# Kernel optimization log

Measured on AMD Instinct MI355X. Metric: run time of the kernel, lower is better.

## Reference

```python
import jax, jax.numpy as jnp
import numpy as np

N_NODES = 100000
N_EDGES = 1600000
N_GRAPHS = 64
D_IN = 64
D_HID = 64
D_OUT = 64


def gcn_conv(x, W, b, src, dst, n):
    """PyG-style GCNConv: x' = D^-1/2 (A+I) D^-1/2 (x W) + b."""
    xw = x @ W  # [N, d_out]
    loops = jnp.arange(n, dtype=src.dtype)
    s = jnp.concatenate([src, loops])  # add self-loops
    d = jnp.concatenate([dst, loops])
    deg = jax.ops.segment_sum(jnp.ones_like(d, dtype=xw.dtype), d, num_segments=n)
    dinv = jax.lax.rsqrt(jnp.maximum(deg, 1.0))
    coef = dinv[s] * dinv[d]  # [E+N]
    msg = xw[s] * coef[:, None]  # gather + scale, [E+N, d_out]
    out = jax.ops.segment_sum(msg, d, num_segments=n)  # scatter-add
    return out + b


def global_mean_pool(h, batch, num_graphs):
    sums = jax.ops.segment_sum(h, batch, num_segments=num_graphs)
    cnt = jax.ops.segment_sum(jnp.ones((h.shape[0],), h.dtype), batch, num_segments=num_graphs)
    return sums / jnp.maximum(cnt, 1.0)[:, None]


def setup_inputs() -> dict:
    key = jax.random.key(0)
    ks = jax.random.split(key, 8)
    x = jax.random.normal(ks[0], (N_NODES, D_IN), dtype=jnp.float32)
    edge_index = jax.random.randint(ks[1], (2, N_EDGES), 0, N_NODES, dtype=jnp.int64 if jax.config.jax_enable_x64 else jnp.int32)
    batch = jnp.sort(jax.random.randint(ks[2], (N_NODES,), 0, N_GRAPHS))
    sc = lambda fan_in: 1.0 / np.sqrt(fan_in)
    W1 = jax.random.uniform(ks[3], (D_IN, D_HID), jnp.float32, -sc(D_IN), sc(D_IN))
    b1 = jnp.zeros((D_HID,), jnp.float32)
    W2 = jax.random.uniform(ks[4], (D_HID, D_HID), jnp.float32, -sc(D_HID), sc(D_HID))
    b2 = jnp.zeros((D_HID,), jnp.float32)
    Wp = jax.random.uniform(ks[5], (D_HID, D_OUT), jnp.float32, -sc(D_HID), sc(D_HID))
    bp = jax.random.uniform(ks[6], (D_OUT,), jnp.float32, -sc(D_HID), sc(D_HID))
    return {"x": x, "edge_index": edge_index, "batch": batch,
            "W1": W1, "b1": b1, "W2": W2, "b2": b2, "Wp": Wp, "bp": bp}


def reference(x, edge_index, batch, W1, b1, W2, b2, Wp, bp):
    src, dst = edge_index[0], edge_index[1]
    n = x.shape[0]
    h = jax.nn.relu(gcn_conv(x, W1, b1, src, dst, n))
    h = jax.nn.relu(gcn_conv(h, W2, b2, src, dst, n))
    hg = global_mean_pool(h, batch, N_GRAPHS)  # [G, d_hid]
    return hg @ Wp + bp  # [G, d_out]
```

## Files before the change

### kernel.cpp

```cpp
#include <hip/hip_runtime.h>
#include <hip/hip_fp16.h>


#define DF 64
#define BSH 7
#define BNODES 128
#define CAP 4096

struct alignas(8)  h4 { __half2 a, b; };
struct alignas(16) h8 { __half2 a, b, c, d; };


__global__ __launch_bounds__(256) void part_kernel(
        const int* __restrict__ src, const int* __restrict__ dst,
        const int4* __restrict__ src4, const int4* __restrict__ dst4,
        int E, unsigned* __restrict__ bedges, int* __restrict__ bucketCur, int nb) {
    __shared__ int lcnt[1024];
    __shared__ int lbase[1024];
    int tid = threadIdx.x;
    for (int t = tid; t < nb; t += 256) lcnt[t] = 0;
    __syncthreads();
    int nq = E >> 2;
    unsigned packed[32];
    int bkt[32];
    int rk[32];
    int qbase = blockIdx.x * 2048;
#pragma unroll
    for (int c = 0; c < 8; c++) {
        int qi = qbase + c * 256 + tid;
        int4 s = {0, 0, 0, 0}, d = {0, 0, 0, 0};
        bool v = qi < nq;
        if (v) { s = src4[qi]; d = dst4[qi]; }
        packed[4*c+0] = (unsigned)s.x | ((unsigned)(d.x & (BNODES-1)) << 24);
        packed[4*c+1] = (unsigned)s.y | ((unsigned)(d.y & (BNODES-1)) << 24);
        packed[4*c+2] = (unsigned)s.z | ((unsigned)(d.z & (BNODES-1)) << 24);
        packed[4*c+3] = (unsigned)s.w | ((unsigned)(d.w & (BNODES-1)) << 24);
        bkt[4*c+0] = v ? (d.x >> BSH) : -1;
        bkt[4*c+1] = v ? (d.y >> BSH) : -1;
        bkt[4*c+2] = v ? (d.z >> BSH) : -1;
        bkt[4*c+3] = v ? (d.w >> BSH) : -1;
    }
#pragma unroll
    for (int j = 0; j < 32; j++)
        rk[j] = (bkt[j] >= 0) ? atomicAdd(&lcnt[bkt[j]], 1) : 0;
    __syncthreads();
    for (int t = tid; t < nb; t += 256)
        lbase[t] = lcnt[t] ? atomicAdd(&bucketCur[t], lcnt[t]) : 0;
    __syncthreads();
#pragma unroll
    for (int j = 0; j < 32; j++) {
        if (bkt[j] >= 0) {
            int pos = lbase[bkt[j]] + rk[j];
            if (pos < CAP) bedges[(size_t)bkt[j] * CAP + pos] = packed[j];
        }
    }
    if (blockIdx.x == 0 && tid < (E & 3)) {
        int e = nq * 4 + tid;
        int sv = src[e], dv = dst[e];
        int b = dv >> BSH;
        int pos = atomicAdd(&bucketCur[b], 1);
        if (pos < CAP)
            bedges[(size_t)b * CAP + pos] =
                (unsigned)sv | ((unsigned)(dv & (BNODES-1)) << 24);
    }
}

__global__ void part_scalar_kernel(const int* __restrict__ src, const int* __restrict__ dst,
                                   int E, unsigned* __restrict__ bedges,
                                   int* __restrict__ bucketCur) {
    int stride = gridDim.x * blockDim.x;
    for (int e = blockIdx.x * blockDim.x + threadIdx.x; e < E; e += stride) {
        int sv = src[e], dv = dst[e];
        int b = dv >> BSH;
        int pos = atomicAdd(&bucketCur[b], 1);
        if (pos < CAP)
            bedges[(size_t)b * CAP + pos] =
                (unsigned)sv | ((unsigned)(dv & (BNODES-1)) << 24);
    }
}


__global__ __launch_bounds__(256) void sort_kernel(
        unsigned* __restrict__ bedges, const int* __restrict__ bucketCur,
        int* __restrict__ offs, float* __restrict__ dinv, int N) {
    __shared__ unsigned ein[CAP];
    __shared__ unsigned eout[CAP];
    __shared__ int cnt[BNODES];
    __shared__ int sc[BNODES];
    __shared__ int off[BNODES + 1];
    __shared__ int cur[BNODES];
    int b = blockIdx.x, tid = threadIdx.x;
    int n = min(bucketCur[b], CAP);
    unsigned* gp = bedges + (size_t)b * CAP;
    if (tid < BNODES) cnt[tid] = 0;
    __syncthreads();
    for (int i = tid; i < n; i += 256) {
        unsigned u = gp[i];
        ein[i] = u;
        atomicAdd(&cnt[u >> 24], 1);
    }
    __syncthreads();
    if (tid < BNODES) sc[tid] = cnt[tid];
    __syncthreads();
    for (int d = 1; d < BNODES; d <<= 1) {
        int v = (tid >= d && tid < BNODES) ? sc[tid - d] : 0;
        __syncthreads();
        if (tid < BNODES) sc[tid] += v;
        __syncthreads();
    }
    if (tid < BNODES) {
        off[tid + 1] = sc[tid];
        cur[tid] = sc[tid] - cnt[tid];
        if (tid == 0) off[0] = 0;
    }
    __syncthreads();
    for (int i = tid; i < n; i += 256) {
        unsigned u = ein[i];
        int p = atomicAdd(&cur[u >> 24], 1);
        eout[p] = u;
    }
    __syncthreads();
    for (int i = tid; i < n; i += 256) gp[i] = eout[i];
    if (tid <= BNODES) offs[(size_t)b * (BNODES + 1) + tid] = off[tid];
    int node = (b << BSH) + tid;
    if (tid < BNODES && node < N)
        dinv[node] = 1.0f / sqrtf((float)(cnt[tid] + 1));
}


__global__ void gemm_f32in(const float4* __restrict__ X4, const float4* __restrict__ W4,
                           const float* __restrict__ dinv, h4* __restrict__ Y2, int n) {
    __shared__ float4 Wl4[64][16];
    __shared__ float Xl[16][68];
    int tid = threadIdx.x;
    float4* Wf = &Wl4[0][0];
#pragma unroll
    for (int i = 0; i < 4; i++) {
        int idx = tid + i * 256;
        Wf[idx] = W4[idx];
    }
    int row0 = blockIdx.x * 16;
    int r = tid >> 4, c4 = tid & 15;
    {
        int row = row0 + r;
        float4 v = (row < n) ? X4[(size_t)row * 16 + c4] : float4{0.f, 0.f, 0.f, 0.f};
        Xl[r][c4 * 4 + 0] = v.x;
        Xl[r][c4 * 4 + 1] = v.y;
        Xl[r][c4 * 4 + 2] = v.z;
        Xl[r][c4 * 4 + 3] = v.w;
    }
    __syncthreads();
    float ax = 0.f, ay = 0.f, az = 0.f, aw = 0.f;
#pragma unroll
    for (int k = 0; k < 64; k++) {
        float xv = Xl[r][k];
        float4 w = Wl4[k][c4];
        ax += xv * w.x;
        ay += xv * w.y;
        az += xv * w.z;
        aw += xv * w.w;
    }
    int row = row0 + r;
    if (row < n) {
        float dv = dinv[row];
        h4 o;
        o.a = __floats2half2_rn(ax * dv, ay * dv);
        o.b = __floats2half2_rn(az * dv, aw * dv);
        Y2[(size_t)row * 16 + c4] = o;
    }
}

__global__ void gemm_f16in(const h4* __restrict__ X2, const float4* __restrict__ W4,
                           const float* __restrict__ dinv, h4* __restrict__ Y2, int n) {
    __shared__ float4 Wl4[64][16];
    __shared__ float Xl[16][68];
    int tid = threadIdx.x;
    float4* Wf = &Wl4[0][0];
#pragma unroll
    for (int i = 0; i < 4; i++) {
        int idx = tid + i * 256;
        Wf[idx] = W4[idx];
    }
    int row0 = blockIdx.x * 16;
    int r = tid >> 4, c4 = tid & 15;
    {
        int row = row0 + r;
        h4 hv = (row < n) ? X2[(size_t)row * 16 + c4] : h4{__half2{0, 0}, __half2{0, 0}};
        float2 va = __half22float2(hv.a), vb = __half22float2(hv.b);
        Xl[r][c4 * 4 + 0] = va.x;
        Xl[r][c4 * 4 + 1] = va.y;
        Xl[r][c4 * 4 + 2] = vb.x;
        Xl[r][c4 * 4 + 3] = vb.y;
    }
    __syncthreads();
    float ax = 0.f, ay = 0.f, az = 0.f, aw = 0.f;
#pragma unroll
    for (int k = 0; k < 64; k++) {
        float xv = Xl[r][k];
        float4 w = Wl4[k][c4];
        ax += xv * w.x;
        ay += xv * w.y;
        az += xv * w.z;
        aw += xv * w.w;
    }
    int row = row0 + r;
    if (row < n) {
        float dv = dinv[row];
        h4 o;
        o.a = __floats2half2_rn(ax * dv, ay * dv);
        o.b = __floats2half2_rn(az * dv, aw * dv);
        Y2[(size_t)row * 16 + c4] = o;
    }
}

#define ACC8(A, w)                                        \
    { float2 _p = __half22float2((w).a);                  \
      A[0] += _p.x; A[1] += _p.y;                         \
      _p = __half22float2((w).b);                         \
      A[2] += _p.x; A[3] += _p.y;                         \
      _p = __half22float2((w).c);                         \
      A[4] += _p.x; A[5] += _p.y;                         \
      _p = __half22float2((w).d);                         \
      A[6] += _p.x; A[7] += _p.y; }

__global__ __launch_bounds__(256) void agg_kernel(
        const h8* __restrict__ Y8, const unsigned* __restrict__ bedges,
        const int* __restrict__ offs, const float* __restrict__ dinv,
        const float* __restrict__ bias, h8* __restrict__ H8, int N) {
    __shared__ unsigned eb[CAP];
    __shared__ int off[65];
    int blk = blockIdx.x;
    int b = blk >> 1, half = blk & 1;
    int tid = threadIdx.x;
    if (tid < 65) off[tid] = offs[(size_t)b * (BNODES + 1) + half * 64 + tid];
    __syncthreads();
    int e0 = off[0];
    int ecnt = off[64] - e0;
    const unsigned* gp = bedges + (size_t)b * CAP + e0;
    for (int i = tid; i < ecnt; i += 256) eb[i] = gp[i];
    __syncthreads();
    int gg = tid >> 3, q = tid & 7;
    float bq[8];
#pragma unroll
    for (int j = 0; j < 8; j++) bq[j] = bias[q * 8 + j];
#pragma unroll
    for (int rr = 0; rr < 2; rr++) {
        int r = gg + rr * 32;
        int s = off[r] - e0, e = off[r + 1] - e0;
        float A0[8], A1[8], A2[8], A3[8];
#pragma unroll
        for (int j = 0; j < 8; j++) { A0[j] = 0.f; A1[j] = 0.f; A2[j] = 0.f; A3[j] = 0.f; }
        int i = s;
        for (; i + 3 < e; i += 4) {
            unsigned u0 = eb[i], u1 = eb[i + 1], u2 = eb[i + 2], u3 = eb[i + 3];
            h8 w0 = Y8[(size_t)(u0 & 0xFFFFFFu) * 8 + q];
            h8 w1 = Y8[(size_t)(u1 & 0xFFFFFFu) * 8 + q];
            h8 w2 = Y8[(size_t)(u2 & 0xFFFFFFu) * 8 + q];
            h8 w3 = Y8[(size_t)(u3 & 0xFFFFFFu) * 8 + q];
            ACC8(A0, w0); ACC8(A1, w1); ACC8(A2, w2); ACC8(A3, w3);
        }
        for (; i < e; i++) {
            unsigned u = eb[i];
            h8 w = Y8[(size_t)(u & 0xFFFFFFu) * 8 + q];
            ACC8(A0, w);
        }
        int node = (b << BSH) + half * 64 + r;
        if (node < N) {
            h8 sv = Y8[(size_t)node * 8 + q];
            float S[8];
            ACC8(A0, sv);
#pragma unroll
            for (int j = 0; j < 8; j++) S[j] = A0[j] + A1[j] + A2[j] + A3[j];
            float dv = dinv[node];
#pragma unroll
            for (int j = 0; j < 8; j++) S[j] = fmaxf(dv * S[j] + bq[j], 0.f);
            h8 o;
            o.a = __floats2half2_rn(S[0], S[1]);
            o.b = __floats2half2_rn(S[2], S[3]);
            o.c = __floats2half2_rn(S[4], S[5]);
            o.d = __floats2half2_rn(S[6], S[7]);
            H8[(size_t)node * 8 + q] = o;
        }
    }
}


__global__ void pool_kernel(const h4* __restrict__ H2, const int* __restrict__ batch,
                            float* __restrict__ sums, int* __restrict__ cnts, int n) {
    int gw = (blockIdx.x * blockDim.x + threadIdx.x) >> 6;
    int lane = threadIdx.x & 63;
    int g = lane >> 4, q = lane & 15;
    int start = gw * 256;
    if (start >= n) return;
    int end = min(start + 256, n);
    float ax = 0.f, ay = 0.f, az = 0.f, aw = 0.f;
    int cur = -1, run = 0;
    for (int i = start + g; i < end; i += 4) {
        int b = batch[i];
        if (b != cur) {
            if (run > 0) {
                atomicAdd(&sums[cur * DF + q * 4 + 0], ax);
                atomicAdd(&sums[cur * DF + q * 4 + 1], ay);
                atomicAdd(&sums[cur * DF + q * 4 + 2], az);
                atomicAdd(&sums[cur * DF + q * 4 + 3], aw);
                if (q == 0) atomicAdd(&cnts[cur], run);
            }
            cur = b; run = 0;
            ax = ay = az = aw = 0.f;
        }
        h4 hv = H2[(size_t)i * 16 + q];
        float2 va = __half22float2(hv.a), vb = __half22float2(hv.b);
        ax += va.x; ay += va.y; az += vb.x; aw += vb.y;
        run++;
    }
    if (run > 0) {
        atomicAdd(&sums[cur * DF + q * 4 + 0], ax);
        atomicAdd(&sums[cur * DF + q * 4 + 1], ay);
        atomicAdd(&sums[cur * DF + q * 4 + 2], az);
        atomicAdd(&sums[cur * DF + q * 4 + 3], aw);
        if (q == 0) atomicAdd(&cnts[cur], run);
    }
}

__global__ void final_kernel(const float* __restrict__ sums, const int* __restrict__ cnts,
                             const float* __restrict__ Wp, const float* __restrict__ bp,
                             float* __restrict__ out) {
    int g = blockIdx.x, j = threadIdx.x;
    __shared__ float hg[64];
    float c = fmaxf((float)cnts[g], 1.f);
    hg[j] = sums[g * DF + j] / c;
    __syncthreads();
    float acc = bp[j];
#pragma unroll
    for (int k = 0; k < 64; k++) acc += hg[k] * Wp[k * DF + j];
    out[g * DF + j] = acc;
}


extern "C" void kernel_launch(void* const* d_in, const int* in_sizes, int n_in,
                              void* d_out, int out_size, void* d_ws, size_t ws_size,
                              hipStream_t stream) {
    const float* x     = (const float*)d_in[0];
    const int*   ei    = (const int*)d_in[1];
    const int*   batch = (const int*)d_in[2];
    const float* W1    = (const float*)d_in[3];
    const float* b1    = (const float*)d_in[4];
    const float* W2    = (const float*)d_in[5];
    const float* b2    = (const float*)d_in[6];
    const float* Wp    = (const float*)d_in[7];
    const float* bp    = (const float*)d_in[8];

    int N = in_sizes[0] / DF;
    int E = in_sizes[1] / 2;
    const int* src = ei;
    const int* dst = ei + E;
    int NB = (N + BNODES - 1) >> BSH;
    int quadOK = ((E & 3) == 0) && (((uintptr_t)ei & 15) == 0) && (((uintptr_t)dst & 15) == 0);

    char* ws = (char*)d_ws;
    auto alloc = [&](size_t bytes) {
        void* p = (void*)ws;
        ws += (bytes + 255) / 256 * 256;
        return p;
    };
    size_t zBucketCur = 0;
    size_t zPsums     = ((size_t)NB * 4 + 255) / 256 * 256;
    size_t zPcnt      = zPsums + 64 * DF * 4;
    size_t zTotal     = zPcnt + 256;
    char*     zbase     = (char*)alloc(zTotal);
    int*      bucketCur = (int*)(zbase + zBucketCur);
    float*    psums     = (float*)(zbase + zPsums);
    int*      pcnt      = (int*)(zbase + zPcnt);

    float*    dinv      = (float*)alloc((size_t)N * 4);
    unsigned* bedges    = (unsigned*)alloc((size_t)NB * CAP * 4);
    int*      offs      = (int*)alloc((size_t)NB * (BNODES + 1) * 4);
    h4*       y2        = (h4*)alloc((size_t)N * DF * 2);
    h4*       h2        = (h4*)alloc((size_t)N * DF * 2);

    hipMemsetAsync(zbase, 0, zTotal, stream);

    if (quadOK) {
        int nq = E >> 2;
        int pblocks = (nq + 2047) / 2048;
        part_kernel<<<pblocks, 256, 0, stream>>>(src, dst, (const int4*)src, (const int4*)dst,
                                                 E, bedges, bucketCur, NB);
    } else {
        part_scalar_kernel<<<1024, 256, 0, stream>>>(src, dst, E, bedges, bucketCur);
    }
    sort_kernel<<<NB, 256, 0, stream>>>(bedges, bucketCur, offs, dinv, N);

    gemm_f32in<<<(N + 15) / 16, 256, 0, stream>>>((const float4*)x, (const float4*)W1, dinv,
                                                  y2, N);
    agg_kernel<<<2 * NB, 256, 0, stream>>>((const h8*)y2, bedges, offs, dinv,
                                           b1, (h8*)h2, N);
    gemm_f16in<<<(N + 15) / 16, 256, 0, stream>>>(h2, (const float4*)W2, dinv,
                                                  y2, N);
    agg_kernel<<<2 * NB, 256, 0, stream>>>((const h8*)y2, bedges, offs, dinv,
                                           b2, (h8*)h2, N);

    int waves = (N + 255) / 256;
    pool_kernel<<<(waves + 3) / 4, 256, 0, stream>>>(h2, batch, psums, pcnt, N);
    final_kernel<<<64, 64, 0, stream>>>(psums, pcnt, Wp, bp, (float*)d_out);
}
```

Baseline: 242.7 us.

## Fuse second aggregation with mean pooling and widen edge gather unroll

The second GCN aggregation now accumulates per-graph sums directly into the pooled buffers, which removes the separate pool kernel and the write and re-read of the hidden activations. The edge gather loop is unrolled to 8 loads in flight so more random gathers overlap. The partition kernel moves to 512-thread blocks, each thread handling 16 edges instead of 32. In exchange, the fused kernel issues more global float atomics, because each 2-node thread group flushes its own per-graph partial sums.

```diff
diff --git a/kernel.cpp b/kernel.cpp
--- a/kernel.cpp
+++ b/kernel.cpp
@@ -11,23 +11,23 @@
 struct alignas(16) h8 { __half2 a, b, c, d; };
 
 
-__global__ __launch_bounds__(256) void part_kernel(
+__global__ __launch_bounds__(512) void part_kernel(
         const int* __restrict__ src, const int* __restrict__ dst,
         const int4* __restrict__ src4, const int4* __restrict__ dst4,
         int E, unsigned* __restrict__ bedges, int* __restrict__ bucketCur, int nb) {
     __shared__ int lcnt[1024];
     __shared__ int lbase[1024];
     int tid = threadIdx.x;
-    for (int t = tid; t < nb; t += 256) lcnt[t] = 0;
+    for (int t = tid; t < nb; t += 512) lcnt[t] = 0;
     __syncthreads();
     int nq = E >> 2;
-    unsigned packed[32];
-    int bkt[32];
-    int rk[32];
+    unsigned packed[16];
+    int bkt[16];
+    int rk[16];
     int qbase = blockIdx.x * 2048;
 #pragma unroll
-    for (int c = 0; c < 8; c++) {
-        int qi = qbase + c * 256 + tid;
+    for (int c = 0; c < 4; c++) {
+        int qi = qbase + c * 512 + tid;
         int4 s = {0, 0, 0, 0}, d = {0, 0, 0, 0};
         bool v = qi < nq;
         if (v) { s = src4[qi]; d = dst4[qi]; }
@@ -41,14 +41,14 @@
         bkt[4*c+3] = v ? (d.w >> BSH) : -1;
     }
 #pragma unroll
-    for (int j = 0; j < 32; j++)
+    for (int j = 0; j < 16; j++)
         rk[j] = (bkt[j] >= 0) ? atomicAdd(&lcnt[bkt[j]], 1) : 0;
     __syncthreads();
-    for (int t = tid; t < nb; t += 256)
+    for (int t = tid; t < nb; t += 512)
         lbase[t] = lcnt[t] ? atomicAdd(&bucketCur[t], lcnt[t]) : 0;
     __syncthreads();
 #pragma unroll
-    for (int j = 0; j < 32; j++) {
+    for (int j = 0; j < 16; j++) {
         if (bkt[j] >= 0) {
             int pos = lbase[bkt[j]] + rk[j];
             if (pos < CAP) bedges[(size_t)bkt[j] * CAP + pos] = packed[j];
@@ -223,6 +223,43 @@
       _p = __half22float2((w).d);                         \
       A[6] += _p.x; A[7] += _p.y; }
 
+#define EDGE_SUM(S_, s_, e_)                                                   \
+    float A0[8], A1[8], A2[8], A3[8];                                          \
+    _Pragma("unroll")                                                          \
+    for (int j = 0; j < 8; j++) { A0[j] = 0.f; A1[j] = 0.f; A2[j] = 0.f; A3[j] = 0.f; } \
+    {                                                                          \
+        int i = (s_);                                                          \
+        for (; i + 7 < (e_); i += 8) {                                         \
+            unsigned u0 = eb[i],     u1 = eb[i + 1], u2 = eb[i + 2], u3 = eb[i + 3]; \
+            unsigned u4 = eb[i + 4], u5 = eb[i + 5], u6 = eb[i + 6], u7 = eb[i + 7]; \
+            h8 w0 = Y8[(size_t)(u0 & 0xFFFFFFu) * 8 + q];                      \
+            h8 w1 = Y8[(size_t)(u1 & 0xFFFFFFu) * 8 + q];                      \
+            h8 w2 = Y8[(size_t)(u2 & 0xFFFFFFu) * 8 + q];                      \
+            h8 w3 = Y8[(size_t)(u3 & 0xFFFFFFu) * 8 + q];                      \
+            h8 w4 = Y8[(size_t)(u4 & 0xFFFFFFu) * 8 + q];                      \
+            h8 w5 = Y8[(size_t)(u5 & 0xFFFFFFu) * 8 + q];                      \
+            h8 w6 = Y8[(size_t)(u6 & 0xFFFFFFu) * 8 + q];                      \
+            h8 w7 = Y8[(size_t)(u7 & 0xFFFFFFu) * 8 + q];                      \
+            ACC8(A0, w0); ACC8(A1, w1); ACC8(A2, w2); ACC8(A3, w3);            \
+            ACC8(A0, w4); ACC8(A1, w5); ACC8(A2, w6); ACC8(A3, w7);            \
+        }                                                                      \
+        for (; i + 3 < (e_); i += 4) {                                         \
+            unsigned u0 = eb[i], u1 = eb[i + 1], u2 = eb[i + 2], u3 = eb[i + 3]; \
+            h8 w0 = Y8[(size_t)(u0 & 0xFFFFFFu) * 8 + q];                      \
+            h8 w1 = Y8[(size_t)(u1 & 0xFFFFFFu) * 8 + q];                      \
+            h8 w2 = Y8[(size_t)(u2 & 0xFFFFFFu) * 8 + q];                      \
+            h8 w3 = Y8[(size_t)(u3 & 0xFFFFFFu) * 8 + q];                      \
+            ACC8(A0, w0); ACC8(A1, w1); ACC8(A2, w2); ACC8(A3, w3);            \
+        }                                                                      \
+        for (; i < (e_); i++) {                                                \
+            unsigned u = eb[i];                                                \
+            h8 w = Y8[(size_t)(u & 0xFFFFFFu) * 8 + q];                        \
+            ACC8(A0, w);                                                       \
+        }                                                                      \
+    }                                                                          \
+    _Pragma("unroll")                                                          \
+    for (int j = 0; j < 8; j++) S_[j] = A0[j] + A1[j] + A2[j] + A3[j];
+
 __global__ __launch_bounds__(256) void agg_kernel(
         const h8* __restrict__ Y8, const unsigned* __restrict__ bedges,
         const int* __restrict__ offs, const float* __restrict__ dinv,
@@ -246,81 +283,88 @@
 #pragma unroll
     for (int rr = 0; rr < 2; rr++) {
         int r = gg + rr * 32;
+        int node = (b << BSH) + half * 64 + r;
+        if (node >= N) continue;
         int s = off[r] - e0, e = off[r + 1] - e0;
-        float A0[8], A1[8], A2[8], A3[8];
-#pragma unroll
-        for (int j = 0; j < 8; j++) { A0[j] = 0.f; A1[j] = 0.f; A2[j] = 0.f; A3[j] = 0.f; }
-        int i = s;
-        for (; i + 3 < e; i += 4) {
-            unsigned u0 = eb[i], u1 = eb[i + 1], u2 = eb[i + 2], u3 = eb[i + 3];
-            h8 w0 = Y8[(size_t)(u0 & 0xFFFFFFu) * 8 + q];
-            h8 w1 = Y8[(size_t)(u1 & 0xFFFFFFu) * 8 + q];
-            h8 w2 = Y8[(size_t)(u2 & 0xFFFFFFu) * 8 + q];
-            h8 w3 = Y8[(size_t)(u3 & 0xFFFFFFu) * 8 + q];
-            ACC8(A0, w0); ACC8(A1, w1); ACC8(A2, w2); ACC8(A3, w3);
+        float S[8];
+        EDGE_SUM(S, s, e);
+        h8 sv = Y8[(size_t)node * 8 + q];
+        ACC8(S, sv);
+        float dv = dinv[node];
+        h8 o;
+        float t0 = fmaxf(dv * S[0] + bq[0], 0.f), t1 = fmaxf(dv * S[1] + bq[1], 0.f);
+        float t2 = fmaxf(dv * S[2] + bq[2], 0.f), t3 = fmaxf(dv * S[3] + bq[3], 0.f);
+        float t4 = fmaxf(dv * S[4] + bq[4], 0.f), t5 = fmaxf(dv * S[5] + bq[5], 0.f);
+        float t6 = fmaxf(dv * S[6] + bq[6], 0.f), t7 = fmaxf(dv * S[7] + bq[7], 0.f);
+        o.a = __floats2half2_rn(t0, t1);
+        o.b = __floats2half2_rn(t2, t3);
+        o.c = __floats2half2_rn(t4, t5);
+        o.d = __floats2half2_rn(t6, t7);
+        H8[(size_t)node * 8 + q] = o;
+    }
+}
+
+__global__ __launch_bounds__(256) void agg_pool_kernel(
+        const h8* __restrict__ Y8, const unsigned* __restrict__ bedges,
+        const int* __restrict__ offs, const float* __restrict__ dinv,
+        const float* __restrict__ bias, const int* __restrict__ batch,
+        float* __restrict__ psums, int* __restrict__ pcnt, int N) {
+    __shared__ unsigned eb[CAP];
+    __shared__ int off[65];
+    int blk = blockIdx.x;
+    int b = blk >> 1, half = blk & 1;
+    int tid = threadIdx.x;
+    if (tid < 65) off[tid] = offs[(size_t)b * (BNODES + 1) + half * 64 + tid];
+    __syncthreads();
+    int e0 = off[0];
+    int ecnt = off[64] - e0;
+    const unsigned* gp = bedges + (size_t)b * CAP + e0;
+    for (int i = tid; i < ecnt; i += 256) eb[i] = gp[i];
+    __syncthreads();
+    int gg = tid >> 3, q = tid & 7;
+    float bq[8];
+#pragma unroll
+    for (int j = 0; j < 8; j++) bq[j] = bias[q * 8 + j];
+    float P[8];
+#pragma unroll
+    for (int j = 0; j < 8; j++) P[j] = 0.f;
+    int curg = -1, pc = 0;
+#pragma unroll
+    for (int rr = 0; rr < 2; rr++) {
+        int r = gg * 2 + rr;
+        int node = (b << BSH) + half * 64 + r;
+        if (node >= N) continue;
+        int s = off[r] - e0, e = off[r + 1] - e0;
+        float S[8];
+        EDGE_SUM(S, s, e);
+        h8 sv = Y8[(size_t)node * 8 + q];
+        ACC8(S, sv);
+        float dv = dinv[node];
+#pragma unroll
+        for (int j = 0; j < 8; j++) S[j] = fmaxf(dv * S[j] + bq[j], 0.f);
+        int bg = batch[node];
+        if (bg != curg) {
+            if (curg >= 0) {
+#pragma unroll
+                for (int j = 0; j < 8; j++) atomicAdd(&psums[curg * DF + q * 8 + j], P[j]);
+                if (q == 0) atomicAdd(&pcnt[curg], pc);
+            }
+#pragma unroll
+            for (int j = 0; j < 8; j++) P[j] = S[j];
+            curg = bg; pc = 1;
+        } else {
+#pragma unroll
+            for (int j = 0; j < 8; j++) P[j] += S[j];
+            pc++;
         }
-        for (; i < e; i++) {
-            unsigned u = eb[i];
-            h8 w = Y8[(size_t)(u & 0xFFFFFFu) * 8 + q];
-            ACC8(A0, w);
-        }
-        int node = (b << BSH) + half * 64 + r;
-        if (node < N) {
-            h8 sv = Y8[(size_t)node * 8 + q];
-            float S[8];
-            ACC8(A0, sv);
-#pragma unroll
-            for (int j = 0; j < 8; j++) S[j] = A0[j] + A1[j] + A2[j] + A3[j];
-            float dv = dinv[node];
-#pragma unroll
-            for (int j = 0; j < 8; j++) S[j] = fmaxf(dv * S[j] + bq[j], 0.f);
-            h8 o;
-            o.a = __floats2half2_rn(S[0], S[1]);
-            o.b = __floats2half2_rn(S[2], S[3]);
-            o.c = __floats2half2_rn(S[4], S[5]);
-            o.d = __floats2half2_rn(S[6], S[7]);
-            H8[(size_t)node * 8 + q] = o;
-        }
-    }
-}
-
-
-__global__ void pool_kernel(const h4* __restrict__ H2, const int* __restrict__ batch,
-                            float* __restrict__ sums, int* __restrict__ cnts, int n) {
-    int gw = (blockIdx.x * blockDim.x + threadIdx.x) >> 6;
-    int lane = threadIdx.x & 63;
-    int g = lane >> 4, q = lane & 15;
-    int start = gw * 256;
-    if (start >= n) return;
-    int end = min(start + 256, n);
-    float ax = 0.f, ay = 0.f, az = 0.f, aw = 0.f;
-    int cur = -1, run = 0;
-    for (int i = start + g; i < end; i += 4) {
-        int b = batch[i];
-        if (b != cur) {
-            if (run > 0) {
-                atomicAdd(&sums[cur * DF + q * 4 + 0], ax);
-                atomicAdd(&sums[cur * DF + q * 4 + 1], ay);
-                atomicAdd(&sums[cur * DF + q * 4 + 2], az);
-                atomicAdd(&sums[cur * DF + q * 4 + 3], aw);
-                if (q == 0) atomicAdd(&cnts[cur], run);
-            }
-            cur = b; run = 0;
-            ax = ay = az = aw = 0.f;
-        }
-        h4 hv = H2[(size_t)i * 16 + q];
-        float2 va = __half22float2(hv.a), vb = __half22float2(hv.b);
-        ax += va.x; ay += va.y; az += vb.x; aw += vb.y;
-        run++;
-    }
-    if (run > 0) {
-        atomicAdd(&sums[cur * DF + q * 4 + 0], ax);
-        atomicAdd(&sums[cur * DF + q * 4 + 1], ay);
-        atomicAdd(&sums[cur * DF + q * 4 + 2], az);
-        atomicAdd(&sums[cur * DF + q * 4 + 3], aw);
-        if (q == 0) atomicAdd(&cnts[cur], run);
-    }
-}
+    }
+    if (curg >= 0) {
+#pragma unroll
+        for (int j = 0; j < 8; j++) atomicAdd(&psums[curg * DF + q * 8 + j], P[j]);
+        if (q == 0) atomicAdd(&pcnt[curg], pc);
+    }
+}
+
 
 __global__ void final_kernel(const float* __restrict__ sums, const int* __restrict__ cnts,
                              const float* __restrict__ Wp, const float* __restrict__ bp,
@@ -363,12 +407,11 @@
         ws += (bytes + 255) / 256 * 256;
         return p;
     };
-    size_t zBucketCur = 0;
-    size_t zPsums     = ((size_t)NB * 4 + 255) / 256 * 256;
-    size_t zPcnt      = zPsums + 64 * DF * 4;
-    size_t zTotal     = zPcnt + 256;
+    size_t zPsums = ((size_t)NB * 4 + 255) / 256 * 256;
+    size_t zPcnt  = zPsums + 64 * DF * 4;
+    size_t zTotal = zPcnt + 256;
     char*     zbase     = (char*)alloc(zTotal);
-    int*      bucketCur = (int*)(zbase + zBucketCur);
+    int*      bucketCur = (int*)zbase;
     float*    psums     = (float*)(zbase + zPsums);
     int*      pcnt      = (int*)(zbase + zPcnt);
 
@@ -383,7 +426,7 @@
     if (quadOK) {
         int nq = E >> 2;
         int pblocks = (nq + 2047) / 2048;
-        part_kernel<<<pblocks, 256, 0, stream>>>(src, dst, (const int4*)src, (const int4*)dst,
+        part_kernel<<<pblocks, 512, 0, stream>>>(src, dst, (const int4*)src, (const int4*)dst,
                                                  E, bedges, bucketCur, NB);
     } else {
         part_scalar_kernel<<<1024, 256, 0, stream>>>(src, dst, E, bedges, bucketCur);
@@ -396,10 +439,8 @@
                                            b1, (h8*)h2, N);
     gemm_f16in<<<(N + 15) / 16, 256, 0, stream>>>(h2, (const float4*)W2, dinv,
                                                   y2, N);
-    agg_kernel<<<2 * NB, 256, 0, stream>>>((const h8*)y2, bedges, offs, dinv,
-                                           b2, (h8*)h2, N);
-
-    int waves = (N + 255) / 256;
-    pool_kernel<<<(waves + 3) / 4, 256, 0, stream>>>(h2, batch, psums, pcnt, N);
+    agg_pool_kernel<<<2 * NB, 256, 0, stream>>>((const h8*)y2, bedges, offs, dinv,
+                                                b2, batch, psums, pcnt, N);
+
     final_kernel<<<64, 64, 0, stream>>>(psums, pcnt, Wp, bp, (float*)d_out);
 }
```

Measured after the change: 689.2 us. 2.84x slower.
